# Optimization experiments

Hardware: AMD Instinct MI355X
Metric: run time of the kernel (lower is better)

Reference implementation:

```python
import jax, jax.numpy as jnp
import numpy as np

D_MODEL, D_K, D_V = 1024, 128, 128
B, S = 4, 2048

def setup_inputs() -> dict:
    key = jax.random.key(0)
    k1, k2, k3, k4 = jax.random.split(key, 4)
    return {
        "x_q": jax.random.normal(k1, (B, S, D_MODEL), dtype=jnp.float32),
        "w_q": jax.random.normal(k2, (D_MODEL, D_K), dtype=jnp.float32),
        "w_k": jax.random.normal(k3, (D_MODEL, D_K), dtype=jnp.float32),
        "w_v": jax.random.normal(k4, (D_MODEL, D_V), dtype=jnp.float32),
    }

def reference(x_q, w_q, w_k, w_v):
    # Self-attention: x_k = x_v = x_q (module defaults)
    Q = x_q @ w_q            # [B,S,d_k]
    K = x_q @ w_k            # [B,S,d_k]
    V = x_q @ w_v            # [B,S,d_v]
    scores = jnp.einsum('bqd,bkd->bqk', Q, K) / jnp.sqrt(jnp.float32(D_K))
    # causal mask: tril (row i attends to cols j <= i)
    causal = jnp.tril(jnp.ones((S, S), dtype=bool))
    scores = jnp.where(causal, scores, -jnp.inf)
    # NOTE: softmax over dim=-2 (query axis), per original module
    attention = jax.nn.softmax(scores, axis=-2)
    out = jnp.einsum('bqk,bkv->bqv', attention, V)
    return out, attention
```

## Files before the change

kernel.cpp:

```cpp
#include <hip/hip_runtime.h>
#include <math.h>
#include <stdint.h>

#define B_ 4
#define S_ 2048
#define DM_ 1024
#define DK_ 128

static constexpr float SCALE = 0.08838834764831845f;

typedef __attribute__((ext_vector_type(8))) short short8;
typedef __attribute__((ext_vector_type(4))) float f32x4;
typedef __attribute__((ext_vector_type(4))) unsigned short us4;

__device__ __forceinline__ unsigned enc_f32(float f){
  unsigned u = __float_as_uint(f);
  return (u & 0x80000000u) ? ~u : (u | 0x80000000u);
}
__device__ __forceinline__ float dec_f32(unsigned u){
  unsigned v = (u & 0x80000000u) ? (u & 0x7FFFFFFFu) : ~u;
  return __uint_as_float(v);
}
__device__ __forceinline__ float f4get(const float4& v, int i){
  switch(i){ case 0: return v.x; case 1: return v.y; case 2: return v.z; default: return v.w; }
}
__device__ __forceinline__ unsigned short bf16rne(float f){
  unsigned u = __float_as_uint(f);
  unsigned r = (u + 0x7FFFu + ((u>>16)&1u)) >> 16;
  return (unsigned short)r;
}
__device__ __forceinline__ float bf16tof(unsigned short h){
  return __uint_as_float((unsigned)h << 16);
}
__device__ __forceinline__ void gload16(const void* g, void* l){
  __builtin_amdgcn_global_load_lds(
      (const __attribute__((address_space(1))) void*)g,
      (__attribute__((address_space(3))) void*)l, 16, 0, 0);
}

__global__ __launch_bounds__(256) void init_kernel(unsigned* __restrict__ cmax){
  int i = blockIdx.x*256 + threadIdx.x;
  if(i < B_*S_) cmax[i] = 0x007FFFFFu;
}

__global__ __launch_bounds__(256) void wconv_kernel(
    const float* __restrict__ Wq, const float* __restrict__ Wk, const float* __restrict__ Wv,
    unsigned short* __restrict__ Wth, unsigned short* __restrict__ Wtl)
{
  const int t = blockIdx.x;
  const int which = blockIdx.y;
  const float* W = (which==0) ? Wq : ((which==1) ? Wk : Wv);
  const int tid = threadIdx.x;
  const size_t obase = ((size_t)which*32 + t)*5120;
  #pragma unroll
  for(int it=0; it<2; ++it){
    int idx = tid + 256*it;
    int col = idx & 127, g = idx >> 7;
    unsigned short hs[8], ls[8];
    #pragma unroll
    for(int j=0;j<8;j++){
      float f = W[(size_t)(t*32 + g*8 + j)*DK_ + col];
      unsigned short h = bf16rne(f);
      hs[j] = h;
      ls[j] = bf16rne(f - bf16tof(h));
    }
    size_t o = obase + (size_t)col*40 + g*8;
    *(us4*)&Wth[o]   = us4{hs[0],hs[1],hs[2],hs[3]};
    *(us4*)&Wth[o+4] = us4{hs[4],hs[5],hs[6],hs[7]};
    *(us4*)&Wtl[o]   = us4{ls[0],ls[1],ls[2],ls[3]};
    *(us4*)&Wtl[o+4] = us4{ls[4],ls[5],ls[6],ls[7]};
  }
}

__global__ __launch_bounds__(256) void qkv_mfma_kernel(
    const float* __restrict__ X,
    const unsigned short* __restrict__ Wth, const unsigned short* __restrict__ Wtl,
    unsigned short* __restrict__ Qh, unsigned short* __restrict__ Ql,
    unsigned short* __restrict__ Kh, unsigned short* __restrict__ Kl,
    unsigned short* __restrict__ Vth, unsigned short* __restrict__ Vtl)
{
  __shared__ __align__(16) unsigned char smem[46080];
  unsigned short* Ah = (unsigned short*)smem;
  unsigned short* Al = (unsigned short*)(smem + 2560);
  const int tid = threadIdx.x;
  const int w = tid >> 6, lane = tid & 63;
  const int which = blockIdx.y;
  const int m0 = blockIdx.x * 32;
  const unsigned char* Wh8 = (const unsigned char*)(Wth + (size_t)which*32*5120);
  const unsigned char* Wl8 = (const unsigned char*)(Wtl + (size_t)which*32*5120);

  const int xrow = tid >> 3, xkq = tid & 7;
  const float* Xg = X + (size_t)(m0 + xrow)*DM_ + xkq*4;
  float4 xv = *reinterpret_cast<const float4*>(Xg);

  #pragma unroll
  for(int ii=0; ii<5; ++ii){
    int i = w + 4*ii;
    const unsigned char* src = (i<10) ? (Wh8 + i*1024) : (Wl8 + (i-10)*1024);
    unsigned dst = (i<10) ? (5120u + i*1024u) : (25600u + (unsigned)(i-10)*1024u);
    gload16(src + lane*16, smem + dst);
  }

  f32x4 acc[4] = {f32x4{0,0,0,0},f32x4{0,0,0,0},f32x4{0,0,0,0},f32x4{0,0,0,0}};
  const int r = w >> 1, c0 = (w & 1)*4;
  const int g = lane >> 4;
  const int aoff = (r*16 + (lane&15))*40 + g*8;
  int buf = 0;
  for(int t=0; t<32; ++t){
    __syncthreads();
    {
      unsigned short h0=bf16rne(xv.x), h1=bf16rne(xv.y), h2=bf16rne(xv.z), h3=bf16rne(xv.w);
      us4 hs = {h0,h1,h2,h3};
      us4 ls = { bf16rne(xv.x - bf16tof(h0)), bf16rne(xv.y - bf16tof(h1)),
                 bf16rne(xv.z - bf16tof(h2)), bf16rne(xv.w - bf16tof(h3)) };
      *(us4*)&Ah[xrow*40 + xkq*4] = hs;
      *(us4*)&Al[xrow*40 + xkq*4] = ls;
    }
    __syncthreads();
    if(t+1 < 32){
      const unsigned char* WhT = Wh8 + (size_t)(t+1)*10240;
      const unsigned char* WlT = Wl8 + (size_t)(t+1)*10240;
      unsigned bhN = (buf^1) ? 15360u : 5120u;
      unsigned blN = (buf^1) ? 35840u : 25600u;
      #pragma unroll
      for(int ii=0; ii<5; ++ii){
        int i = w + 4*ii;
        const unsigned char* src = (i<10) ? (WhT + i*1024) : (WlT + (i-10)*1024);
        unsigned dst = (i<10) ? (bhN + i*1024) : (blN + (unsigned)(i-10)*1024);
        gload16(src + lane*16, smem + dst);
      }
      xv = *reinterpret_cast<const float4*>(Xg + (t+1)*32);
    }
    const unsigned short* Bhc = (const unsigned short*)(smem + (buf ? 15360 : 5120));
    const unsigned short* Blc = (const unsigned short*)(smem + (buf ? 35840 : 25600));
    short8 ah = *(const short8*)&Ah[aoff];
    short8 al = *(const short8*)&Al[aoff];
    #pragma unroll
    for(int c=0;c<4;c++){
      int boff = ((c0+c)*16 + (lane&15))*40 + g*8;
      short8 bh = *(const short8*)&Bhc[boff];
      short8 bl = *(const short8*)&Blc[boff];
      acc[c] = __builtin_amdgcn_mfma_f32_16x16x32_bf16(ah, bh, acc[c], 0, 0, 0);
      acc[c] = __builtin_amdgcn_mfma_f32_16x16x32_bf16(ah, bl, acc[c], 0, 0, 0);
      acc[c] = __builtin_amdgcn_mfma_f32_16x16x32_bf16(al, bh, acc[c], 0, 0, 0);
    }
    buf ^= 1;
  }
  const int b = m0 >> 11;
  const int orow0 = (lane>>4)*4;
  if(which != 2){
    unsigned short* Oh = (which==0) ? Qh : Kh;
    unsigned short* Ol = (which==0) ? Ql : Kl;
    #pragma unroll
    for(int c=0;c<4;c++){
      int col = (c0+c)*16 + (lane&15);
      #pragma unroll
      for(int j=0;j<4;j++){
        float f = acc[c][j];
        unsigned short h = bf16rne(f);
        unsigned short lo = bf16rne(f - bf16tof(h));
        size_t o = (size_t)(m0 + r*16 + orow0 + j)*DK_ + col;
        Oh[o] = h; Ol[o] = lo;
      }
    }
  } else {
    __syncthreads();
    float* Tmp = (float*)smem;
    #pragma unroll
    for(int c=0;c<4;c++){
      int col = (c0+c)*16 + (lane&15);
      #pragma unroll
      for(int j=0;j<4;j++)
        Tmp[(r*16 + orow0 + j)*133 + col] = acc[c][j];
    }
    __syncthreads();
    const int s0 = m0 & (S_-1);
    #pragma unroll
    for(int l2=0;l2<16;l2++){
      int p = tid + 256*l2;
      int d = p >> 5, rr = p & 31;
      float f = Tmp[rr*133 + d];
      unsigned short h = bf16rne(f);
      Vth[(size_t)(b*DK_ + d)*S_ + s0 + rr] = h;
      Vtl[(size_t)(b*DK_ + d)*S_ + s0 + rr] = bf16rne(f - bf16tof(h));
    }
  }
}

__global__ __launch_bounds__(256) void scores_kernel(
    const unsigned short* __restrict__ Qh, const unsigned short* __restrict__ Ql,
    const unsigned short* __restrict__ Kh, const unsigned short* __restrict__ Kl,
    float* __restrict__ attn, unsigned* __restrict__ cmax)
{
  const int tj = blockIdx.x, ti = blockIdx.y, b = blockIdx.z;
  const int tid = threadIdx.x;
  const int q0 = ti*64, k0 = tj*64;
  if(tj > ti){
    float4 z = {0.f,0.f,0.f,0.f};
    #pragma unroll
    for(int l=0;l<4;l++){
      int p = tid + 256*l;
      int r = p >> 4, c = (p & 15) << 2;
      *reinterpret_cast<float4*>(&attn[((size_t)(b*S_) + q0 + r)*S_ + k0 + c]) = z;
    }
    return;
  }
  __shared__ __align__(16) unsigned short sm[18432];
  __shared__ float cred[16][64];
  unsigned short* Qhs = sm;
  unsigned short* Qls = sm + 4608;
  unsigned short* Khs = sm + 9216;
  unsigned short* Kls = sm + 13824;
  const int w = tid >> 6, lane = tid & 63, l15 = lane & 15, g = lane >> 4;
  f32x4 acc[4] = {f32x4{0,0,0,0},f32x4{0,0,0,0},f32x4{0,0,0,0},f32x4{0,0,0,0}};
  for(int kh=0; kh<2; ++kh){
    __syncthreads();
    #pragma unroll
    for(int l=0;l<2;l++){
      int p = tid + 256*l;
      int row = p >> 3, cc = p & 7;
      size_t gq = (size_t)(b*S_ + q0 + row)*DK_ + kh*64 + cc*8;
      size_t gk = (size_t)(b*S_ + k0 + row)*DK_ + kh*64 + cc*8;
      int lo_ = row*72 + cc*8;
      *(short8*)&Qhs[lo_] = *(const short8*)&Qh[gq];
      *(short8*)&Qls[lo_] = *(const short8*)&Ql[gq];
      *(short8*)&Khs[lo_] = *(const short8*)&Kh[gk];
      *(short8*)&Kls[lo_] = *(const short8*)&Kl[gk];
    }
    __syncthreads();
    #pragma unroll
    for(int ks=0; ks<2; ++ks){
      int ao = (w*16 + l15)*72 + ks*32 + g*8;
      short8 ah = *(const short8*)&Qhs[ao];
      short8 al = *(const short8*)&Qls[ao];
      #pragma unroll
      for(int c=0;c<4;c++){
        int bo = (c*16 + l15)*72 + ks*32 + g*8;
        short8 bh = *(const short8*)&Khs[bo];
        short8 bl = *(const short8*)&Kls[bo];
        acc[c] = __builtin_amdgcn_mfma_f32_16x16x32_bf16(ah, bh, acc[c], 0, 0, 0);
        acc[c] = __builtin_amdgcn_mfma_f32_16x16x32_bf16(ah, bl, acc[c], 0, 0, 0);
        acc[c] = __builtin_amdgcn_mfma_f32_16x16x32_bf16(al, bh, acc[c], 0, 0, 0);
      }
    }
  }
  const bool full = (ti > tj);
  const int qbase = q0 + w*16 + g*4;
  #pragma unroll
  for(int c=0;c<4;c++){
    int kcol = k0 + c*16 + l15;
    float cm = -INFINITY;
    #pragma unroll
    for(int j=0;j<4;j++){
      int q = qbase + j;
      float s = acc[c][j]*SCALE;
      bool valid = full || (q >= kcol);
      attn[((size_t)(b*S_) + q)*S_ + kcol] = valid ? s : 0.f;
      if(valid) cm = fmaxf(cm, s);
    }
    cred[w*4 + g][c*16 + l15] = cm;
  }
  __syncthreads();
  if(tid < 64){
    float m = cred[0][tid];
    #pragma unroll
    for(int gg=1;gg<16;gg++) m = fmaxf(m, cred[gg][tid]);
    atomicMax(&cmax[b*S_ + k0 + tid], enc_f32(m));
  }
}

__global__ __launch_bounds__(256) void expsum_kernel(
    const float* __restrict__ attn, const unsigned* __restrict__ cmax,
    float* __restrict__ colpart)
{
  const int cj = blockIdx.x, ti = blockIdx.y, b = blockIdx.z;
  if(ti < 4*cj) return;
  __shared__ float part[4][256];
  const int tid = threadIdx.x;
  const int c4 = tid & 63, g = tid >> 6;
  const int q0 = ti*64, k0 = cj*256;
  const int kbase = k0 + c4*4;
  float mc[4];
  #pragma unroll
  for(int j=0;j<4;j++) mc[j] = dec_f32(cmax[b*S_ + kbase + j]);
  float sum[4] = {0.f,0.f,0.f,0.f};
  #pragma unroll 4
  for(int rr=0;rr<16;rr++){
    int q = q0 + g*16 + rr;
    size_t idx = ((size_t)(b*S_) + q)*S_ + kbase;
    float4 sv = *reinterpret_cast<const float4*>(&attn[idx]);
    sum[0] += (q >= kbase+0) ? __expf(sv.x - mc[0]) : 0.f;
    sum[1] += (q >= kbase+1) ? __expf(sv.y - mc[1]) : 0.f;
    sum[2] += (q >= kbase+2) ? __expf(sv.z - mc[2]) : 0.f;
    sum[3] += (q >= kbase+3) ? __expf(sv.w - mc[3]) : 0.f;
  }
  #pragma unroll
  for(int j=0;j<4;j++) part[g][c4*4+j] = sum[j];
  __syncthreads();
  {
    int k = k0 + tid;
    float tot = ((part[0][tid] + part[1][tid]) + part[2][tid]) + part[3][tid];
    colpart[((size_t)(b*S_) + k)*32 + ti] = tot;
  }
}

__global__ __launch_bounds__(256) void colreduce_kernel(
    const float* __restrict__ colpart, float* __restrict__ rcol)
{
  int i = blockIdx.x*256 + threadIdx.x;
  if(i >= B_*S_) return;
  int k = i & (S_-1);
  int t0 = k >> 6;
  float s = 0.f;
  for(int t=t0; t<32; t++) s += colpart[(size_t)i*32 + t];
  rcol[i] = 1.0f / s;
}

__global__ __launch_bounds__(256) void pv_kernel(
    float* __restrict__ attn, const unsigned* __restrict__ cmax,
    const float* __restrict__ rcol,
    const unsigned short* __restrict__ Vth, const unsigned short* __restrict__ Vtl,
    float* __restrict__ part, int ns)
{
  __shared__ __align__(16) unsigned short sm[27648];
  unsigned short* Ahs = sm;
  unsigned short* Als = sm + 4608;
  unsigned short* Vhs = sm + 9216;
  unsigned short* Vls = sm + 18432;
  const int b = blockIdx.z, tid = threadIdx.x;
  const int sp = blockIdx.y;
  const int w = tid >> 6, lane = tid & 63, l15 = lane & 15, g = lane >> 4;
  const int t = 31 - (int)blockIdx.x;
  const int q0 = t*64;
  const int nch = t + 1;
  const int lo = (sp*nch)/ns, hi = ((sp+1)*nch)/ns;
  f32x4 acc[8] = {f32x4{0,0,0,0},f32x4{0,0,0,0},f32x4{0,0,0,0},f32x4{0,0,0,0},
                  f32x4{0,0,0,0},f32x4{0,0,0,0},f32x4{0,0,0,0},f32x4{0,0,0,0}};
  const int er = tid >> 4, ekq = (tid & 15) << 2;
  for(int ch=lo; ch<hi; ++ch){
    const int k0c = ch*64;
    uint4 mu = *reinterpret_cast<const uint4*>(&cmax[b*S_ + k0c + ekq]);
    float4 r4 = *reinterpret_cast<const float4*>(&rcol[b*S_ + k0c + ekq]);
    float mc0 = dec_f32(mu.x), mc1 = dec_f32(mu.y), mc2 = dec_f32(mu.z), mc3 = dec_f32(mu.w);
    const bool diag = (ch == t);
    __syncthreads();
    #pragma unroll
    for(int rr=0; rr<4; ++rr){
      int row = rr*16 + er;
      size_t ea = ((size_t)(b*S_) + q0 + row)*S_ + k0c + ekq;
      float4 sv = *reinterpret_cast<const float4*>(&attn[ea]);
      float p0 = __expf(sv.x - mc0)*r4.x;
      float p1 = __expf(sv.y - mc1)*r4.y;
      float p2 = __expf(sv.z - mc2)*r4.z;
      float p3 = __expf(sv.w - mc3)*r4.w;
      if(diag){
        p0 = (row >= ekq+0) ? p0 : 0.f;
        p1 = (row >= ekq+1) ? p1 : 0.f;
        p2 = (row >= ekq+2) ? p2 : 0.f;
        p3 = (row >= ekq+3) ? p3 : 0.f;
      }
      float4 pv4 = {p0,p1,p2,p3};
      *reinterpret_cast<float4*>(&attn[ea]) = pv4;
      unsigned short h0=bf16rne(p0), h1=bf16rne(p1), h2=bf16rne(p2), h3=bf16rne(p3);
      *(us4*)&Ahs[row*72 + ekq] = us4{h0,h1,h2,h3};
      *(us4*)&Als[row*72 + ekq] = us4{ bf16rne(p0-bf16tof(h0)), bf16rne(p1-bf16tof(h1)),
                                       bf16rne(p2-bf16tof(h2)), bf16rne(p3-bf16tof(h3)) };
    }
    #pragma unroll
    for(int v=0; v<4; ++v){
      int idx = v*256 + tid;
      int d = idx >> 3, c8 = (idx & 7) << 3;
      size_t ga = (size_t)(b*DK_ + d)*S_ + k0c + c8;
      *(short8*)&Vhs[d*72 + c8] = *(const short8*)&Vth[ga];
      *(short8*)&Vls[d*72 + c8] = *(const short8*)&Vtl[ga];
    }
    __syncthreads();
    #pragma unroll
    for(int ks=0; ks<2; ++ks){
      int ao = (w*16 + l15)*72 + ks*32 + g*8;
      short8 ah = *(const short8*)&Ahs[ao];
      short8 al = *(const short8*)&Als[ao];
      #pragma unroll
      for(int c=0;c<8;c++){
        int bo = (c*16 + l15)*72 + ks*32 + g*8;
        short8 bh = *(const short8*)&Vhs[bo];
        short8 bl = *(const short8*)&Vls[bo];
        acc[c] = __builtin_amdgcn_mfma_f32_16x16x32_bf16(ah, bh, acc[c], 0, 0, 0);
        acc[c] = __builtin_amdgcn_mfma_f32_16x16x32_bf16(ah, bl, acc[c], 0, 0, 0);
        acc[c] = __builtin_amdgcn_mfma_f32_16x16x32_bf16(al, bh, acc[c], 0, 0, 0);
      }
    }
  }
  float* pout = part + (((size_t)(sp*B_ + b))*S_ + q0)*DK_;
  #pragma unroll
  for(int c=0;c<8;c++){
    #pragma unroll
    for(int j=0;j<4;j++){
      int qrow = w*16 + g*4 + j;
      pout[(size_t)qrow*DK_ + c*16 + l15] = acc[c][j];
    }
  }
}

__global__ __launch_bounds__(256) void pvreduce_kernel(
    const float* __restrict__ part, float* __restrict__ out, int ns)
{
  const int N4 = (B_*S_*DK_)/4;
  int i = blockIdx.x*256 + threadIdx.x;
  if(i >= N4) return;
  const float4* p = reinterpret_cast<const float4*>(part);
  float4 a = p[i];
  for(int s=1; s<ns; ++s){
    float4 q = p[(size_t)s*N4 + i];
    a.x += q.x; a.y += q.y; a.z += q.z; a.w += q.w;
  }
  reinterpret_cast<float4*>(out)[i] = a;
}

extern "C" void kernel_launch(void* const* d_in, const int* in_sizes, int n_in,
                              void* d_out, int out_size, void* d_ws, size_t ws_size,
                              hipStream_t stream)
{
  (void)in_sizes; (void)n_in; (void)out_size;
  const float* X  = (const float*)d_in[0];
  const float* Wq = (const float*)d_in[1];
  const float* Wk = (const float*)d_in[2];
  const float* Wv = (const float*)d_in[3];
  float* out  = (float*)d_out;
  float* attn = out + (size_t)B_*S_*DK_;

  float* ws = (float*)d_ws;
  unsigned* cmax = (unsigned*)ws;
  float* rcol    = ws + 8192;
  float* colpart = ws + 16384;
  unsigned short* Wth = (unsigned short*)(ws + 278528);
  unsigned short* Wtl = (unsigned short*)(ws + 524288);
  unsigned short* Qh  = (unsigned short*)(ws + 770048);
  unsigned short* Ql  = (unsigned short*)(ws + 1294336);
  unsigned short* Kh  = (unsigned short*)(ws + 1818624);
  unsigned short* Kl  = (unsigned short*)(ws + 2342912);
  unsigned short* Vth = (unsigned short*)(ws + 2867200);
  unsigned short* Vtl = (unsigned short*)(ws + 3391488);
  const size_t base = 3915776;
  float* part    = ws + base;

  int ns = 4;
  if(ws_size < (base + (size_t)4*1048576)*sizeof(float)) ns = 2;
  if(ws_size < (base + (size_t)2*1048576)*sizeof(float)) ns = 1;

  init_kernel<<<dim3(32), dim3(256), 0, stream>>>(cmax);
  wconv_kernel<<<dim3(32,3), dim3(256), 0, stream>>>(Wq, Wk, Wv, Wth, Wtl);
  qkv_mfma_kernel<<<dim3(256,3), dim3(256), 0, stream>>>(X, Wth, Wtl, Qh, Ql, Kh, Kl, Vth, Vtl);
  scores_kernel<<<dim3(32,32,4), dim3(256), 0, stream>>>(Qh, Ql, Kh, Kl, attn, cmax);
  expsum_kernel<<<dim3(8,32,4), dim3(256), 0, stream>>>(attn, cmax, colpart);
  colreduce_kernel<<<dim3(32), dim3(256), 0, stream>>>(colpart, rcol);
  pv_kernel<<<dim3(32,ns,4), dim3(256), 0, stream>>>(attn, cmax, rcol, Vth, Vtl, part, ns);
  pvreduce_kernel<<<dim3(1024), dim3(256), 0, stream>>>(part, out, ns);
}
```

Measured before the change: 118.5 us.

## Double QKV projection M-tile to 64 rows per block for weight reuse

The QKV projection kernel now computes 64 rows per block instead of 32, with each wave holding two 16-row fragments that share every loaded B (weight) fragment. This halves the number of blocks and the total weight traffic from global memory into LDS, raising MFMA work per LDS load. The V transpose epilogue is split into two half-tile passes so it still fits the shared buffer. The cost is fewer blocks (384 instead of 768) and more registers and LDS per block, which may lower occupancy.

```diff
diff --git a/kernel.cpp b/kernel.cpp
--- a/kernel.cpp
+++ b/kernel.cpp
@@ -79,49 +79,53 @@
     unsigned short* __restrict__ Kh, unsigned short* __restrict__ Kl,
     unsigned short* __restrict__ Vth, unsigned short* __restrict__ Vtl)
 {
-  __shared__ __align__(16) unsigned char smem[46080];
+  __shared__ __align__(16) unsigned char smem[51200];
   unsigned short* Ah = (unsigned short*)smem;
-  unsigned short* Al = (unsigned short*)(smem + 2560);
+  unsigned short* Al = (unsigned short*)(smem + 5120);
   const int tid = threadIdx.x;
   const int w = tid >> 6, lane = tid & 63;
+  const int wr = w >> 1, wc = w & 1;
+  const int l15 = lane & 15, g = lane >> 4;
   const int which = blockIdx.y;
-  const int m0 = blockIdx.x * 32;
+  const int m0 = blockIdx.x * 64;
   const unsigned char* Wh8 = (const unsigned char*)(Wth + (size_t)which*32*5120);
   const unsigned char* Wl8 = (const unsigned char*)(Wtl + (size_t)which*32*5120);
 
-  const int xrow = tid >> 3, xkq = tid & 7;
-  const float* Xg = X + (size_t)(m0 + xrow)*DM_ + xkq*4;
-  float4 xv = *reinterpret_cast<const float4*>(Xg);
+  const int R = tid >> 3, kq = tid & 7;
+  const float* Xg0 = X + (size_t)(m0 + R)*DM_ + kq*4;
+  const float* Xg1 = Xg0 + (size_t)32*DM_;
+  float4 xv0 = *reinterpret_cast<const float4*>(Xg0);
+  float4 xv1 = *reinterpret_cast<const float4*>(Xg1);
 
   #pragma unroll
   for(int ii=0; ii<5; ++ii){
     int i = w + 4*ii;
     const unsigned char* src = (i<10) ? (Wh8 + i*1024) : (Wl8 + (i-10)*1024);
-    unsigned dst = (i<10) ? (5120u + i*1024u) : (25600u + (unsigned)(i-10)*1024u);
+    unsigned dst = (i<10) ? (10240u + i*1024u) : (20480u + (unsigned)(i-10)*1024u);
     gload16(src + lane*16, smem + dst);
   }
 
-  f32x4 acc[4] = {f32x4{0,0,0,0},f32x4{0,0,0,0},f32x4{0,0,0,0},f32x4{0,0,0,0}};
-  const int r = w >> 1, c0 = (w & 1)*4;
-  const int g = lane >> 4;
-  const int aoff = (r*16 + (lane&15))*40 + g*8;
+  f32x4 acc[2][4] = {{f32x4{0,0,0,0},f32x4{0,0,0,0},f32x4{0,0,0,0},f32x4{0,0,0,0}},
+                     {f32x4{0,0,0,0},f32x4{0,0,0,0},f32x4{0,0,0,0},f32x4{0,0,0,0}}};
   int buf = 0;
   for(int t=0; t<32; ++t){
     __syncthreads();
     {
-      unsigned short h0=bf16rne(xv.x), h1=bf16rne(xv.y), h2=bf16rne(xv.z), h3=bf16rne(xv.w);
-      us4 hs = {h0,h1,h2,h3};
-      us4 ls = { bf16rne(xv.x - bf16tof(h0)), bf16rne(xv.y - bf16tof(h1)),
-                 bf16rne(xv.z - bf16tof(h2)), bf16rne(xv.w - bf16tof(h3)) };
-      *(us4*)&Ah[xrow*40 + xkq*4] = hs;
-      *(us4*)&Al[xrow*40 + xkq*4] = ls;
+      unsigned short h0=bf16rne(xv0.x), h1=bf16rne(xv0.y), h2=bf16rne(xv0.z), h3=bf16rne(xv0.w);
+      *(us4*)&Ah[R*40 + kq*4] = us4{h0,h1,h2,h3};
+      *(us4*)&Al[R*40 + kq*4] = us4{ bf16rne(xv0.x - bf16tof(h0)), bf16rne(xv0.y - bf16tof(h1)),
+                                     bf16rne(xv0.z - bf16tof(h2)), bf16rne(xv0.w - bf16tof(h3)) };
+      unsigned short k0=bf16rne(xv1.x), k1=bf16rne(xv1.y), k2=bf16rne(xv1.z), k3=bf16rne(xv1.w);
+      *(us4*)&Ah[(R+32)*40 + kq*4] = us4{k0,k1,k2,k3};
+      *(us4*)&Al[(R+32)*40 + kq*4] = us4{ bf16rne(xv1.x - bf16tof(k0)), bf16rne(xv1.y - bf16tof(k1)),
+                                          bf16rne(xv1.z - bf16tof(k2)), bf16rne(xv1.w - bf16tof(k3)) };
     }
     __syncthreads();
     if(t+1 < 32){
       const unsigned char* WhT = Wh8 + (size_t)(t+1)*10240;
       const unsigned char* WlT = Wl8 + (size_t)(t+1)*10240;
-      unsigned bhN = (buf^1) ? 15360u : 5120u;
-      unsigned blN = (buf^1) ? 35840u : 25600u;
+      unsigned bhN = (buf^1) ? 30720u : 10240u;
+      unsigned blN = (buf^1) ? 40960u : 20480u;
       #pragma unroll
       for(int ii=0; ii<5; ++ii){
         int i = w + 4*ii;
@@ -129,60 +133,77 @@
         unsigned dst = (i<10) ? (bhN + i*1024) : (blN + (unsigned)(i-10)*1024);
         gload16(src + lane*16, smem + dst);
       }
-      xv = *reinterpret_cast<const float4*>(Xg + (t+1)*32);
-    }
-    const unsigned short* Bhc = (const unsigned short*)(smem + (buf ? 15360 : 5120));
-    const unsigned short* Blc = (const unsigned short*)(smem + (buf ? 35840 : 25600));
-    short8 ah = *(const short8*)&Ah[aoff];
-    short8 al = *(const short8*)&Al[aoff];
+      xv0 = *reinterpret_cast<const float4*>(Xg0 + (t+1)*32);
+      xv1 = *reinterpret_cast<const float4*>(Xg1 + (t+1)*32);
+    }
+    const unsigned short* Bhc = (const unsigned short*)(smem + (buf ? 30720 : 10240));
+    const unsigned short* Blc = (const unsigned short*)(smem + (buf ? 40960 : 20480));
+    short8 ah0 = *(const short8*)&Ah[(wr*32 + l15)*40 + g*8];
+    short8 al0 = *(const short8*)&Al[(wr*32 + l15)*40 + g*8];
+    short8 ah1 = *(const short8*)&Ah[(wr*32 + 16 + l15)*40 + g*8];
+    short8 al1 = *(const short8*)&Al[(wr*32 + 16 + l15)*40 + g*8];
     #pragma unroll
     for(int c=0;c<4;c++){
-      int boff = ((c0+c)*16 + (lane&15))*40 + g*8;
+      int boff = ((wc*64 + c*16) + l15)*40 + g*8;
       short8 bh = *(const short8*)&Bhc[boff];
       short8 bl = *(const short8*)&Blc[boff];
-      acc[c] = __builtin_amdgcn_mfma_f32_16x16x32_bf16(ah, bh, acc[c], 0, 0, 0);
-      acc[c] = __builtin_amdgcn_mfma_f32_16x16x32_bf16(ah, bl, acc[c], 0, 0, 0);
-      acc[c] = __builtin_amdgcn_mfma_f32_16x16x32_bf16(al, bh, acc[c], 0, 0, 0);
+      acc[0][c] = __builtin_amdgcn_mfma_f32_16x16x32_bf16(ah0, bh, acc[0][c], 0, 0, 0);
+      acc[0][c] = __builtin_amdgcn_mfma_f32_16x16x32_bf16(ah0, bl, acc[0][c], 0, 0, 0);
+      acc[0][c] = __builtin_amdgcn_mfma_f32_16x16x32_bf16(al0, bh, acc[0][c], 0, 0, 0);
+      acc[1][c] = __builtin_amdgcn_mfma_f32_16x16x32_bf16(ah1, bh, acc[1][c], 0, 0, 0);
+      acc[1][c] = __builtin_amdgcn_mfma_f32_16x16x32_bf16(ah1, bl, acc[1][c], 0, 0, 0);
+      acc[1][c] = __builtin_amdgcn_mfma_f32_16x16x32_bf16(al1, bh, acc[1][c], 0, 0, 0);
     }
     buf ^= 1;
   }
   const int b = m0 >> 11;
-  const int orow0 = (lane>>4)*4;
+  const int orow0 = g*4;
   if(which != 2){
     unsigned short* Oh = (which==0) ? Qh : Kh;
     unsigned short* Ol = (which==0) ? Ql : Kl;
     #pragma unroll
-    for(int c=0;c<4;c++){
-      int col = (c0+c)*16 + (lane&15);
+    for(int fr=0;fr<2;fr++){
       #pragma unroll
-      for(int j=0;j<4;j++){
-        float f = acc[c][j];
+      for(int c=0;c<4;c++){
+        int col = wc*64 + c*16 + l15;
+        #pragma unroll
+        for(int j=0;j<4;j++){
+          float f = acc[fr][c][j];
+          unsigned short h = bf16rne(f);
+          unsigned short lo = bf16rne(f - bf16tof(h));
+          size_t o = (size_t)(m0 + wr*32 + fr*16 + orow0 + j)*DK_ + col;
+          Oh[o] = h; Ol[o] = lo;
+        }
+      }
+    }
+  } else {
+    float* Tmp = (float*)smem;
+    const int s0 = m0 & (S_-1);
+    #pragma unroll
+    for(int hr=0; hr<2; ++hr){
+      __syncthreads();
+      if(wr == hr){
+        #pragma unroll
+        for(int fr=0;fr<2;fr++){
+          #pragma unroll
+          for(int c=0;c<4;c++){
+            int col = wc*64 + c*16 + l15;
+            #pragma unroll
+            for(int j=0;j<4;j++)
+              Tmp[(fr*16 + orow0 + j)*133 + col] = acc[fr][c][j];
+          }
+        }
+      }
+      __syncthreads();
+      #pragma unroll
+      for(int l2=0;l2<16;l2++){
+        int p = tid + 256*l2;
+        int d = p >> 5, rr = p & 31;
+        float f = Tmp[rr*133 + d];
         unsigned short h = bf16rne(f);
-        unsigned short lo = bf16rne(f - bf16tof(h));
-        size_t o = (size_t)(m0 + r*16 + orow0 + j)*DK_ + col;
-        Oh[o] = h; Ol[o] = lo;
-      }
-    }
-  } else {
-    __syncthreads();
-    float* Tmp = (float*)smem;
-    #pragma unroll
-    for(int c=0;c<4;c++){
-      int col = (c0+c)*16 + (lane&15);
-      #pragma unroll
-      for(int j=0;j<4;j++)
-        Tmp[(r*16 + orow0 + j)*133 + col] = acc[c][j];
-    }
-    __syncthreads();
-    const int s0 = m0 & (S_-1);
-    #pragma unroll
-    for(int l2=0;l2<16;l2++){
-      int p = tid + 256*l2;
-      int d = p >> 5, rr = p & 31;
-      float f = Tmp[rr*133 + d];
-      unsigned short h = bf16rne(f);
-      Vth[(size_t)(b*DK_ + d)*S_ + s0 + rr] = h;
-      Vtl[(size_t)(b*DK_ + d)*S_ + s0 + rr] = bf16rne(f - bf16tof(h));
+        Vth[(size_t)(b*DK_ + d)*S_ + s0 + hr*32 + rr] = h;
+        Vtl[(size_t)(b*DK_ + d)*S_ + s0 + hr*32 + rr] = bf16rne(f - bf16tof(h));
+      }
     }
   }
 }
@@ -450,7 +471,7 @@
 
   init_kernel<<<dim3(32), dim3(256), 0, stream>>>(cmax);
   wconv_kernel<<<dim3(32,3), dim3(256), 0, stream>>>(Wq, Wk, Wv, Wth, Wtl);
-  qkv_mfma_kernel<<<dim3(256,3), dim3(256), 0, stream>>>(X, Wth, Wtl, Qh, Ql, Kh, Kl, Vth, Vtl);
+  qkv_mfma_kernel<<<dim3(128,3), dim3(256), 0, stream>>>(X, Wth, Wtl, Qh, Ql, Kh, Kl, Vth, Vtl);
   scores_kernel<<<dim3(32,32,4), dim3(256), 0, stream>>>(Qh, Ql, Kh, Kl, attn, cmax);
   expsum_kernel<<<dim3(8,32,4), dim3(256), 0, stream>>>(attn, cmax, colpart);
   colreduce_kernel<<<dim3(32), dim3(256), 0, stream>>>(colpart, rcol);
```

Result: no change. 118.7 us (+0.2%).

## Pre-split X into bf16 hi/lo tiles and async-load them in QKV GEMM

Applied to the files above, without the earlier changes.

Adds a separate kernel that converts X once into bf16 high/low pairs in an MFMA-friendly tiled layout, stored temporarily in the attention output buffer. The QKV GEMM then loads A tiles with global_load_lds double buffering, like the weights. This removes the per-iteration register conversion, the LDS store and one barrier per k-step, and stops X being converted three times (once per Q/K/V). The cost is an extra kernel launch plus a write and re-read of a 64 MB intermediate.

```diff
diff --git a/kernel.cpp b/kernel.cpp
--- a/kernel.cpp
+++ b/kernel.cpp
@@ -21,9 +21,6 @@
   unsigned v = (u & 0x80000000u) ? (u & 0x7FFFFFFFu) : ~u;
   return __uint_as_float(v);
 }
-__device__ __forceinline__ float f4get(const float4& v, int i){
-  switch(i){ case 0: return v.x; case 1: return v.y; case 2: return v.z; default: return v.w; }
-}
 __device__ __forceinline__ unsigned short bf16rne(float f){
   unsigned u = __float_as_uint(f);
   unsigned r = (u + 0x7FFFu + ((u>>16)&1u)) >> 16;
@@ -41,6 +38,31 @@
 __global__ __launch_bounds__(256) void init_kernel(unsigned* __restrict__ cmax){
   int i = blockIdx.x*256 + threadIdx.x;
   if(i < B_*S_) cmax[i] = 0x007FFFFFu;
+}
+
+__global__ __launch_bounds__(256) void xconv_kernel(
+    const float* __restrict__ X,
+    unsigned short* __restrict__ Xth, unsigned short* __restrict__ Xtl)
+{
+  const int kt = blockIdx.x & 31, mb = blockIdx.x >> 5;
+  const int tid = threadIdx.x;
+  const int unit = tid & 127, half = tid >> 7;
+  const int g = unit >> 5, row = unit & 31;
+  const float* src = X + (size_t)(mb*32 + row)*DM_ + kt*32 + g*8;
+  float4 a = *reinterpret_cast<const float4*>(src);
+  float4 b = *reinterpret_cast<const float4*>(src + 4);
+  unsigned short* dst = (half ? Xtl : Xth) + ((size_t)(mb*32 + kt)*128 + unit)*8;
+  if(half == 0){
+    us4 h0 = {bf16rne(a.x),bf16rne(a.y),bf16rne(a.z),bf16rne(a.w)};
+    us4 h1 = {bf16rne(b.x),bf16rne(b.y),bf16rne(b.z),bf16rne(b.w)};
+    *(us4*)dst = h0; *(us4*)(dst+4) = h1;
+  } else {
+    us4 l0 = {bf16rne(a.x - bf16tof(bf16rne(a.x))), bf16rne(a.y - bf16tof(bf16rne(a.y))),
+              bf16rne(a.z - bf16tof(bf16rne(a.z))), bf16rne(a.w - bf16tof(bf16rne(a.w)))};
+    us4 l1 = {bf16rne(b.x - bf16tof(bf16rne(b.x))), bf16rne(b.y - bf16tof(bf16rne(b.y))),
+              bf16rne(b.z - bf16tof(bf16rne(b.z))), bf16rne(b.w - bf16tof(bf16rne(b.w)))};
+    *(us4*)dst = l0; *(us4*)(dst+4) = l1;
+  }
 }
 
 __global__ __launch_bounds__(256) void wconv_kernel(
@@ -73,71 +95,60 @@
 }
 
 __global__ __launch_bounds__(256) void qkv_mfma_kernel(
-    const float* __restrict__ X,
+    const unsigned short* __restrict__ Xth, const unsigned short* __restrict__ Xtl,
     const unsigned short* __restrict__ Wth, const unsigned short* __restrict__ Wtl,
     unsigned short* __restrict__ Qh, unsigned short* __restrict__ Ql,
     unsigned short* __restrict__ Kh, unsigned short* __restrict__ Kl,
     unsigned short* __restrict__ Vth, unsigned short* __restrict__ Vtl)
 {
-  __shared__ __align__(16) unsigned char smem[46080];
-  unsigned short* Ah = (unsigned short*)smem;
-  unsigned short* Al = (unsigned short*)(smem + 2560);
+  __shared__ __align__(16) unsigned char smem[49152];
   const int tid = threadIdx.x;
   const int w = tid >> 6, lane = tid & 63;
+  const int l15 = lane & 15, g = lane >> 4;
   const int which = blockIdx.y;
   const int m0 = blockIdx.x * 32;
+  const int mb = blockIdx.x;
   const unsigned char* Wh8 = (const unsigned char*)(Wth + (size_t)which*32*5120);
   const unsigned char* Wl8 = (const unsigned char*)(Wtl + (size_t)which*32*5120);
-
-  const int xrow = tid >> 3, xkq = tid & 7;
-  const float* Xg = X + (size_t)(m0 + xrow)*DM_ + xkq*4;
-  float4 xv = *reinterpret_cast<const float4*>(Xg);
-
+  const unsigned short* Asrc = ((w < 2) ? Xth : Xtl) + (size_t)(mb*32)*1024 + (w & 1)*512 + lane*8;
+  const unsigned Adst = (unsigned)((w & 1)*1024) + ((w < 2) ? 0u : 2048u);
+
+  gload16(Asrc, smem + Adst + lane*0  );
   #pragma unroll
   for(int ii=0; ii<5; ++ii){
     int i = w + 4*ii;
     const unsigned char* src = (i<10) ? (Wh8 + i*1024) : (Wl8 + (i-10)*1024);
-    unsigned dst = (i<10) ? (5120u + i*1024u) : (25600u + (unsigned)(i-10)*1024u);
+    unsigned dst = 8192u + ((i<10) ? (unsigned)i*1024u : 10240u + (unsigned)(i-10)*1024u);
     gload16(src + lane*16, smem + dst);
   }
 
   f32x4 acc[4] = {f32x4{0,0,0,0},f32x4{0,0,0,0},f32x4{0,0,0,0},f32x4{0,0,0,0}};
   const int r = w >> 1, c0 = (w & 1)*4;
-  const int g = lane >> 4;
-  const int aoff = (r*16 + (lane&15))*40 + g*8;
+  const int aoff = (g*32 + r*16 + l15)*8;
   int buf = 0;
   for(int t=0; t<32; ++t){
     __syncthreads();
-    {
-      unsigned short h0=bf16rne(xv.x), h1=bf16rne(xv.y), h2=bf16rne(xv.z), h3=bf16rne(xv.w);
-      us4 hs = {h0,h1,h2,h3};
-      us4 ls = { bf16rne(xv.x - bf16tof(h0)), bf16rne(xv.y - bf16tof(h1)),
-                 bf16rne(xv.z - bf16tof(h2)), bf16rne(xv.w - bf16tof(h3)) };
-      *(us4*)&Ah[xrow*40 + xkq*4] = hs;
-      *(us4*)&Al[xrow*40 + xkq*4] = ls;
-    }
-    __syncthreads();
     if(t+1 < 32){
+      gload16(Asrc + (size_t)(t+1)*1024, smem + (buf^1)*4096 + Adst);
       const unsigned char* WhT = Wh8 + (size_t)(t+1)*10240;
       const unsigned char* WlT = Wl8 + (size_t)(t+1)*10240;
-      unsigned bhN = (buf^1) ? 15360u : 5120u;
-      unsigned blN = (buf^1) ? 35840u : 25600u;
+      unsigned bbase = 8192u + (unsigned)(buf^1)*20480u;
       #pragma unroll
       for(int ii=0; ii<5; ++ii){
         int i = w + 4*ii;
         const unsigned char* src = (i<10) ? (WhT + i*1024) : (WlT + (i-10)*1024);
-        unsigned dst = (i<10) ? (bhN + i*1024) : (blN + (unsigned)(i-10)*1024);
+        unsigned dst = bbase + ((i<10) ? (unsigned)i*1024u : 10240u + (unsigned)(i-10)*1024u);
         gload16(src + lane*16, smem + dst);
       }
-      xv = *reinterpret_cast<const float4*>(Xg + (t+1)*32);
-    }
-    const unsigned short* Bhc = (const unsigned short*)(smem + (buf ? 15360 : 5120));
-    const unsigned short* Blc = (const unsigned short*)(smem + (buf ? 35840 : 25600));
-    short8 ah = *(const short8*)&Ah[aoff];
-    short8 al = *(const short8*)&Al[aoff];
+    }
+    const unsigned short* Ab = (const unsigned short*)(smem + buf*4096);
+    const unsigned short* Bhc = (const unsigned short*)(smem + 8192 + buf*20480);
+    const unsigned short* Blc = Bhc + 5120;
+    short8 ah = *(const short8*)&Ab[aoff];
+    short8 al = *(const short8*)&Ab[1024 + aoff];
     #pragma unroll
     for(int c=0;c<4;c++){
-      int boff = ((c0+c)*16 + (lane&15))*40 + g*8;
+      int boff = ((c0+c)*16 + l15)*40 + g*8;
       short8 bh = *(const short8*)&Bhc[boff];
       short8 bl = *(const short8*)&Blc[boff];
       acc[c] = __builtin_amdgcn_mfma_f32_16x16x32_bf16(ah, bh, acc[c], 0, 0, 0);
@@ -147,13 +158,13 @@
     buf ^= 1;
   }
   const int b = m0 >> 11;
-  const int orow0 = (lane>>4)*4;
+  const int orow0 = g*4;
   if(which != 2){
     unsigned short* Oh = (which==0) ? Qh : Kh;
     unsigned short* Ol = (which==0) ? Ql : Kl;
     #pragma unroll
     for(int c=0;c<4;c++){
-      int col = (c0+c)*16 + (lane&15);
+      int col = (c0+c)*16 + l15;
       #pragma unroll
       for(int j=0;j<4;j++){
         float f = acc[c][j];
@@ -168,7 +179,7 @@
     float* Tmp = (float*)smem;
     #pragma unroll
     for(int c=0;c<4;c++){
-      int col = (c0+c)*16 + (lane&15);
+      int col = (c0+c)*16 + l15;
       #pragma unroll
       for(int j=0;j<4;j++)
         Tmp[(r*16 + orow0 + j)*133 + col] = acc[c][j];
@@ -429,6 +440,9 @@
   float* out  = (float*)d_out;
   float* attn = out + (size_t)B_*S_*DK_;
 
+  unsigned short* Xth = (unsigned short*)attn;
+  unsigned short* Xtl = Xth + (size_t)8388608;
+
   float* ws = (float*)d_ws;
   unsigned* cmax = (unsigned*)ws;
   float* rcol    = ws + 8192;
@@ -449,8 +463,9 @@
   if(ws_size < (base + (size_t)2*1048576)*sizeof(float)) ns = 1;
 
   init_kernel<<<dim3(32), dim3(256), 0, stream>>>(cmax);
+  xconv_kernel<<<dim3(8192), dim3(256), 0, stream>>>(X, Xth, Xtl);
   wconv_kernel<<<dim3(32,3), dim3(256), 0, stream>>>(Wq, Wk, Wv, Wth, Wtl);
-  qkv_mfma_kernel<<<dim3(256,3), dim3(256), 0, stream>>>(X, Wth, Wtl, Qh, Ql, Kh, Kl, Vth, Vtl);
+  qkv_mfma_kernel<<<dim3(256,3), dim3(256), 0, stream>>>(Xth, Xtl, Wth, Wtl, Qh, Ql, Kh, Kl, Vth, Vtl);
   scores_kernel<<<dim3(32,32,4), dim3(256), 0, stream>>>(Qh, Ql, Kh, Kl, attn, cmax);
   expsum_kernel<<<dim3(8,32,4), dim3(256), 0, stream>>>(attn, cmax, colpart);
   colreduce_kernel<<<dim3(32), dim3(256), 0, stream>>>(colpart, rcol);
```

Measured after the change: 124.7 us. 5.3% more time.
